# Kernel optimization log

Hardware: AMD Instinct MI355X
Metric: run time of the kernel (lower is better)

Reference implementation:

```python
import jax, jax.numpy as jnp
import numpy as np

DIM = 1024
HEADS = 16
HIDDEN = 4 * DIM

def _gelu_erf(x):
    # GELU via erf, matching the torch module exactly
    return x * 0.5 * (1.0 + jax.lax.erf(x / jnp.sqrt(2.0).astype(x.dtype)))

def setup_inputs() -> dict:
    key = jax.random.key(0)
    ks = jax.random.split(key, 12)
    s = 0.02
    x = jax.random.normal(ks[0], (2, 2048, DIM), dtype=jnp.float32)
    # MHSA params
    ln1_g = jnp.ones((DIM,), jnp.float32)
    ln1_b = jnp.zeros((DIM,), jnp.float32)
    w_qkv = jax.random.normal(ks[1], (DIM, 3 * DIM), jnp.float32) * s  # no bias
    w_proj = jax.random.normal(ks[2], (DIM, DIM), jnp.float32) * s
    b_proj = jnp.zeros((DIM,), jnp.float32)
    # ResMLP params
    ln2_g = jnp.ones((DIM,), jnp.float32)
    ln2_b = jnp.zeros((DIM,), jnp.float32)
    w1 = jax.random.normal(ks[3], (DIM, HIDDEN), jnp.float32) * s
    b1 = jnp.zeros((HIDDEN,), jnp.float32)
    w2 = jax.random.normal(ks[4], (HIDDEN, DIM), jnp.float32) * s
    b2 = jnp.zeros((DIM,), jnp.float32)
    return {"x": x, "ln1_g": ln1_g, "ln1_b": ln1_b, "w_qkv": w_qkv,
            "w_proj": w_proj, "b_proj": b_proj, "ln2_g": ln2_g, "ln2_b": ln2_b,
            "w1": w1, "b1": b1, "w2": w2, "b2": b2}

def _layernorm(x, g, b, eps=1e-5):
    mu = jnp.mean(x, axis=-1, keepdims=True)
    var = jnp.mean(jnp.square(x - mu), axis=-1, keepdims=True)
    return (x - mu) * jax.lax.rsqrt(var + eps) * g + b

def reference(x, ln1_g, ln1_b, w_qkv, w_proj, b_proj, ln2_g, ln2_b, w1, b1, w2, b2):
    B, N, C = x.shape
    H = HEADS
    hd = C // H
    scale = hd ** -0.5
    # --- MHSA (dropout is identity in eval) ---
    h = _layernorm(x, ln1_g, ln1_b)
    qkv = (h @ w_qkv).reshape(B, N, 3, H, hd)
    q = jnp.transpose(qkv[:, :, 0], (0, 2, 1, 3))  # [B,H,N,hd]
    k = jnp.transpose(qkv[:, :, 1], (0, 2, 1, 3))
    v = jnp.transpose(qkv[:, :, 2], (0, 2, 1, 3))
    attn = jax.nn.softmax(jnp.einsum('bhnd,bhmd->bhnm', q, k) * scale, axis=-1)
    out = jnp.einsum('bhnm,bhmd->bhnd', attn, v)
    out = jnp.transpose(out, (0, 2, 1, 3)).reshape(B, N, C)
    x = x + out @ w_proj + b_proj
    # --- ResMLP ---
    h = _layernorm(x, ln2_g, ln2_b)
    h = _gelu_erf(h @ w1 + b1)
    x = x + h @ w2 + b2
    return x
```

## Files before the change

### kernel.cpp

```cpp
#include <hip/hip_runtime.h>
#include <stdint.h>


#define DIMC 1024
#define HIDN 4096
#define SEQ  2048
#define TOK  4096

typedef __bf16 bf16x8 __attribute__((ext_vector_type(8)));
typedef float  f32x4  __attribute__((ext_vector_type(4)));
typedef unsigned short ushort8 __attribute__((ext_vector_type(8)));

__device__ inline unsigned short f2bf(float f) {
  union { float f; unsigned u; } v; v.f = f;
  unsigned u = v.u;
  return (unsigned short)((u + 0x7fffu + ((u >> 16) & 1u)) >> 16);
}

__device__ inline unsigned cvt_pk_bf16(float a, float b) {
  unsigned r;
  asm("v_cvt_pk_bf16_f32 %0, %1, %2" : "=v"(r) : "v"(a), "v"(b));
  return r;
}

#if __has_builtin(__builtin_amdgcn_exp2f)
__device__ inline float fast_exp2(float x) { return __builtin_amdgcn_exp2f(x); }
#else
__device__ inline float fast_exp2(float x) { return exp2f(x); }
#endif

__device__ inline f32x4 mfma_bf16(bf16x8 a, bf16x8 b, f32x4 c) {
  return __builtin_amdgcn_mfma_f32_16x16x32_bf16(a, b, c, 0, 0, 0);
}

typedef const __attribute__((address_space(1))) unsigned int* as1_u32p;
typedef __attribute__((address_space(3))) unsigned int* as3_u32p;
__device__ inline void gload_lds16(const unsigned short* g, unsigned short* l) {
  __builtin_amdgcn_global_load_lds((as1_u32p)(const void*)g, (as3_u32p)(void*)l,
                                   16, 0, 0);
}

__global__ __launch_bounds__(256)
void prep_kernel(const float* __restrict__ wa, unsigned short* __restrict__ ta,
                 const float* __restrict__ wb, unsigned short* __restrict__ tb,
                 const float* __restrict__ wc, unsigned short* __restrict__ tc,
                 const float* __restrict__ wd, unsigned short* __restrict__ td,
                 const float* __restrict__ x, const float* __restrict__ g,
                 const float* __restrict__ bln, unsigned short* __restrict__ out) {
  const int bid = blockIdx.x;
  const int tid = threadIdx.x;
  if (bid < 12288) {
    __shared__ float tile[32][33];
    const float* w; unsigned short* wt; int K, N, bx, by;
    if (bid < 3072)      { w = wa; wt = ta; K = 1024; N = 3072; bx = bid % 96;  by = bid / 96; }
    else if (bid < 4096) { int i = bid - 3072; w = wb; wt = tb; K = 1024; N = 1024; bx = i % 32;  by = i / 32; }
    else if (bid < 8192) { int i = bid - 4096; w = wc; wt = tc; K = 1024; N = 4096; bx = i % 128; by = i / 128; }
    else                 { int i = bid - 8192; w = wd; wt = td; K = 4096; N = 1024; bx = i % 32;  by = i / 32; }
    const int k0 = by * 32;
    const int n0 = bx * 32;
    const int tx = tid & 31;
    const int ty = tid >> 5;
#pragma unroll
    for (int i = 0; i < 4; i++)
      tile[ty + i * 8][tx] = w[(size_t)(k0 + ty + i * 8) * N + n0 + tx];
    __syncthreads();
#pragma unroll
    for (int i = 0; i < 4; i++)
      wt[(size_t)(n0 + ty + i * 8) * K + k0 + tx] = f2bf(tile[tx][ty + i * 8]);
  } else {
    const int row = bid - 12288;
    const float4* xr = (const float4*)&x[(size_t)row * DIMC];
    float4 v = xr[tid];
    float s  = v.x + v.y + v.z + v.w;
    float sq = v.x * v.x + v.y * v.y + v.z * v.z + v.w * v.w;
#pragma unroll
    for (int off = 32; off > 0; off >>= 1) {
      s  += __shfl_xor(s, off, 64);
      sq += __shfl_xor(sq, off, 64);
    }
    __shared__ float red[8];
    if ((tid & 63) == 0) { red[tid >> 6] = s; red[4 + (tid >> 6)] = sq; }
    __syncthreads();
    s  = red[0] + red[1] + red[2] + red[3];
    sq = red[4] + red[5] + red[6] + red[7];
    const float mu  = s * (1.0f / DIMC);
    const float var = sq * (1.0f / DIMC) - mu * mu;
    const float rs  = rsqrtf(var + 1e-5f);
    const int c = tid * 4;
    float vv[4] = {v.x, v.y, v.z, v.w};
#pragma unroll
    for (int j = 0; j < 4; j++)
      out[(size_t)row * DIMC + c + j] = f2bf((vv[j] - mu) * rs * g[c + j] + bln[c + j]);
  }
}

__global__ __launch_bounds__(256)
void ln_kernel(const float* __restrict__ x, const float* __restrict__ g,
               const float* __restrict__ b, unsigned short* __restrict__ out) {
  const int row = blockIdx.x;
  const int tid = threadIdx.x;
  const float4* xr = (const float4*)&x[(size_t)row * DIMC];
  float4 v = xr[tid];
  float s  = v.x + v.y + v.z + v.w;
  float sq = v.x * v.x + v.y * v.y + v.z * v.z + v.w * v.w;
#pragma unroll
  for (int off = 32; off > 0; off >>= 1) {
    s  += __shfl_xor(s, off, 64);
    sq += __shfl_xor(sq, off, 64);
  }
  __shared__ float red[8];
  if ((tid & 63) == 0) { red[tid >> 6] = s; red[4 + (tid >> 6)] = sq; }
  __syncthreads();
  s  = red[0] + red[1] + red[2] + red[3];
  sq = red[4] + red[5] + red[6] + red[7];
  const float mu  = s * (1.0f / DIMC);
  const float var = sq * (1.0f / DIMC) - mu * mu;
  const float rs  = rsqrtf(var + 1e-5f);
  const int c = tid * 4;
  float vv[4] = {v.x, v.y, v.z, v.w};
#pragma unroll
  for (int j = 0; j < 4; j++)
    out[(size_t)row * DIMC + c + j] = f2bf((vv[j] - mu) * rs * g[c + j] + b[c + j]);
}

template <int EPI, int TN>
__global__ __launch_bounds__(256, (TN == 64) ? 4 : 3)
void gemm_bt(const unsigned short* __restrict__ A,
             const unsigned short* __restrict__ Bt,
             float* __restrict__ Cf, unsigned short* __restrict__ Cb,
             const float* __restrict__ bias, const float* __restrict__ res,
             int M, int N, int K,
             unsigned short* __restrict__ qd,
             unsigned short* __restrict__ kTd,
             unsigned short* __restrict__ vd) {
  constexpr int NU = TN / 32;
  constexpr int BP = TN / 32;
  __shared__ unsigned short As[128 * 64];
  __shared__ unsigned short Bs[TN * 64];
  const int gx  = N / TN;
  const int bid = blockIdx.x;
  const int xcd = bid & 7;
  const int lin = bid >> 3;
  const int bx  = lin % gx;
  const int by  = (xcd << 2) + lin / gx;
  const int tid  = threadIdx.x;
  const int lane = tid & 63;
  const int wave = tid >> 6;
  const int m0 = by * 128;
  const int n0 = bx * TN;
  const int wm = (wave >> 1) * 64;
  const int wn = (wave & 1) * (TN / 2);
  const int lm = lane & 15;
  const int lg = lane >> 4;
  const int r8 = tid >> 3;
  const int c8 = tid & 7;
  const int csrc = ((c8 ^ (r8 & 7)) * 8);

  const unsigned short* gA = &A [(size_t)(m0 + r8) * K + csrc];
  const unsigned short* gB = &Bt[(size_t)(n0 + r8) * K + csrc];

  f32x4 acc[4][NU];
#pragma unroll
  for (int t = 0; t < 4; t++)
#pragma unroll
    for (int u = 0; u < NU; u++) acc[t][u] = {0.f, 0.f, 0.f, 0.f};

  const int x0 = (lg ^ (lm & 7)) * 8;
  const int x1 = ((4 + lg) ^ (lm & 7)) * 8;

  for (int k0 = 0; k0 < K; k0 += 64) {
    __syncthreads();
#pragma unroll
    for (int p = 0; p < 4; p++)
      gload_lds16(gA + (size_t)p * 32 * K + k0, &As[p * 2048 + wave * 512]);
#pragma unroll
    for (int p = 0; p < BP; p++)
      gload_lds16(gB + (size_t)p * 32 * K + k0, &Bs[p * 2048 + wave * 512]);
    __syncthreads();
#pragma unroll
    for (int sub = 0; sub < 2; sub++) {
      const int xo = sub ? x1 : x0;
      bf16x8 af[4], bfr[NU];
#pragma unroll
      for (int t = 0; t < 4; t++)  af[t]  = *(const bf16x8*)&As[(wm + t * 16 + lm) * 64 + xo];
#pragma unroll
      for (int u = 0; u < NU; u++) bfr[u] = *(const bf16x8*)&Bs[(wn + u * 16 + lm) * 64 + xo];
#pragma unroll
      for (int t = 0; t < 4; t++)
#pragma unroll
        for (int u = 0; u < NU; u++)
          acc[t][u] = mfma_bf16(af[t], bfr[u], acc[t][u]);
    }
  }

#pragma unroll
  for (int t = 0; t < 4; t++) {
    const int row = m0 + wm + t * 16 + lg * 4;
#pragma unroll
    for (int u = 0; u < NU; u++) {
      const int col = n0 + wn + u * 16 + lm;
#pragma unroll
      for (int r = 0; r < 4; r++) {
        float v = acc[t][u][r];
        size_t idx = (size_t)(row + r) * N + col;
        if (EPI == 0) {
          const int rr = row + r;
          const int bb = rr >> 11, key = rr & (SEQ - 1);
          if (col < 1024) {
            qd[(size_t)rr * 1024 + col] = f2bf(v * 0.18033688011112042f);
          } else if (col < 2048) {
            const int d = col - 1024, h = d >> 6, dd = d & 63;
            kTd[(((size_t)(bb * 16 + h)) * SEQ + key) * 64 + dd] = f2bf(v);
          } else {
            vd[(size_t)rr * 1024 + (col - 2048)] = f2bf(v);
          }
        } else if (EPI == 1) {
          Cf[idx] = v + bias[col] + res[idx];
        } else {
          float xg = v + bias[col];
          Cb[idx] = f2bf(0.5f * xg * (1.0f + erff(xg * 0.70710678118654752f)));
        }
      }
    }
  }
}

__global__ __launch_bounds__(256)
void v_transpose(const unsigned short* __restrict__ vd,
                 unsigned short* __restrict__ vT) {
  const int kt = blockIdx.x;
  const int bh = blockIdx.y;
  const int b = bh >> 4, h = bh & 15;
  const int tid = threadIdx.x;
  __shared__ unsigned short tile[64 * 72];
  const int tok = tid >> 2;
  const int ch  = tid & 3;
  const size_t srow = (size_t)(b * SEQ + kt * 64 + tok) * 1024 + h * 64;
  ushort8 va = *(const ushort8*)&vd[srow + ch * 8];
  ushort8 vb = *(const ushort8*)&vd[srow + 32 + ch * 8];
  *(ushort8*)&tile[tok * 72 + ch * 8] = va;
  *(ushort8*)&tile[tok * 72 + 32 + ch * 8] = vb;
  __syncthreads();
  const int d = tid >> 2;
  ushort8 o0, o1;
#pragma unroll
  for (int j = 0; j < 8; j++) {
    o0[j] = tile[(ch * 8 + j) * 72 + d];
    o1[j] = tile[((ch + 4) * 8 + j) * 72 + d];
  }
  const size_t vdst = ((size_t)bh * 64 + d) * SEQ + kt * 64;
  *(ushort8*)&vT[vdst + ch * 8] = o0;
  *(ushort8*)&vT[vdst + 32 + ch * 8] = o1;
}

__global__ __launch_bounds__(256, 2)
void attn_kernel(const unsigned short* __restrict__ qbuf,
                 const unsigned short* __restrict__ kT,
                 const unsigned short* __restrict__ vT,
                 unsigned short* __restrict__ out) {
  const int bid = blockIdx.x;
  const int xcd = bid & 7;
  const int lin = bid >> 3;
  const int bh  = (xcd << 2) + (lin >> 4);
  const int qt  = lin & 15;
  const int b  = bh >> 4;
  const int h  = bh & 15;
  const int tid  = threadIdx.x;
  const int lane = tid & 63;
  const int wave = tid >> 6;
  const int ks   = wave >> 1;
  const int qh   = wave & 1;
  const int lm = lane & 15;
  const int lg = lane >> 4;

  __shared__ f32x4 shbuf[4096];
  unsigned short* Ks = (unsigned short*)shbuf;
  unsigned short* Vs = (unsigned short*)shbuf + 8192;
  unsigned short* Ps = (unsigned short*)shbuf + 16384;

  const int qrow_base = b * SEQ + qt * 128 + qh * 64;
  bf16x8 qb[4][2];
#pragma unroll
  for (int s = 0; s < 4; s++)
#pragma unroll
    for (int c = 0; c < 2; c++)
      qb[s][c] = *(const bf16x8*)&qbuf[(size_t)(qrow_base + s * 16 + lm) * 1024 +
                                       h * 64 + c * 32 + lg * 8];

  f32x4 o[4][4];
#pragma unroll
  for (int dt = 0; dt < 4; dt++)
#pragma unroll
    for (int s = 0; s < 4; s++) o[dt][s] = {0.f, 0.f, 0.f, 0.f};
  float li[4] = {0.f, 0.f, 0.f, 0.f};

  const unsigned short* kbp = &kT[(size_t)bh * SEQ * 64];
  const unsigned short* vbp = &vT[(size_t)bh * 64 * SEQ];
  const int ts   = tid & 127;
  const int srow = ts >> 3;
  const int slog = ((ts & 7) ^ (srow & 7)) * 8;
  const int koff = ks * 1024;
  const int xk0 = ((lg)     ^ (lm & 7)) * 8;
  const int xk1 = ((4 + lg) ^ (lm & 7)) * 8;
  unsigned short* ksb = Ks + ks * 4096;
  unsigned short* vsb = Vs + ks * 4096;
  unsigned short* psb = Ps + wave * 4096;
  unsigned short* kdst = ksb + ((ts >> 6) * 512);
  unsigned short* vdst = vsb + ((ts >> 6) * 512);

  for (int kt = 0; kt < 16; kt++) {
    __syncthreads();
#pragma unroll
    for (int p = 0; p < 4; p++) {
      gload_lds16(&kbp[(size_t)(koff + kt * 64 + p * 16 + srow) * 64 + slog],
                  kdst + p * 1024);
      gload_lds16(&vbp[(size_t)(p * 16 + srow) * SEQ + koff + kt * 64 + slog],
                  vdst + p * 1024);
    }
    __syncthreads();

#pragma unroll
    for (int u = 0; u < 4; u++) {
      bf16x8 ka0 = *(const bf16x8*)&ksb[(u * 16 + lm) * 64 + xk0];
      bf16x8 ka1 = *(const bf16x8*)&ksb[(u * 16 + lm) * 64 + xk1];
      f32x4 st[4];
#pragma unroll
      for (int s = 0; s < 4; s++) {
        f32x4 z = {0.f, 0.f, 0.f, 0.f};
        z = mfma_bf16(ka0, qb[s][0], z);
        z = mfma_bf16(ka1, qb[s][1], z);
        st[s] = z;
      }
#pragma unroll
      for (int s = 0; s < 4; s++) {
        float p0 = fast_exp2(st[s][0] - 8.0f);
        float p1 = fast_exp2(st[s][1] - 8.0f);
        float p2 = fast_exp2(st[s][2] - 8.0f);
        float p3 = fast_exp2(st[s][3] - 8.0f);
        li[s] += (p0 + p1) + (p2 + p3);
        uint2 pk;
        pk.x = cvt_pk_bf16(p0, p1);
        pk.y = cvt_pk_bf16(p2, p3);
        const int phys = (u * 2 + (lg >> 1)) ^ (lm & 7);
        *(uint2*)&psb[(s * 16 + lm) * 64 + phys * 8 + (lg & 1) * 4] = pk;
      }
    }

#pragma unroll
    for (int kc = 0; kc < 2; kc++) {
      const int xo = kc ? xk1 : xk0;
      bf16x8 pb[4];
#pragma unroll
      for (int s = 0; s < 4; s++)
        pb[s] = *(const bf16x8*)&psb[(s * 16 + lm) * 64 + xo];
#pragma unroll
      for (int dt = 0; dt < 4; dt++) {
        bf16x8 va = *(const bf16x8*)&vsb[(dt * 16 + lm) * 64 + xo];
#pragma unroll
        for (int s = 0; s < 4; s++)
          o[dt][s] = mfma_bf16(va, pb[s], o[dt][s]);
      }
    }
  }

  __syncthreads();
  f32x4* ob = shbuf + qh * 1088;
  float*  lb = (float*)(ob + 1024);
  if (ks == 1) {
#pragma unroll
    for (int dt = 0; dt < 4; dt++)
#pragma unroll
      for (int s = 0; s < 4; s++)
        ob[(dt * 4 + s) * 64 + lane] = o[dt][s];
#pragma unroll
    for (int s = 0; s < 4; s++) lb[s * 64 + lane] = li[s];
  }
  __syncthreads();
  if (ks == 0) {
#pragma unroll
    for (int dt = 0; dt < 4; dt++)
#pragma unroll
      for (int s = 0; s < 4; s++)
        o[dt][s] += ob[(dt * 4 + s) * 64 + lane];
#pragma unroll
    for (int s = 0; s < 4; s++) {
      float l = li[s] + lb[s * 64 + lane];
      l += __shfl_xor(l, 16, 64);
      l += __shfl_xor(l, 32, 64);
      const float inv = 1.0f / l;
#pragma unroll
      for (int dt = 0; dt < 4; dt++) {
        uint2 ok;
        ok.x = cvt_pk_bf16(o[dt][s][0] * inv, o[dt][s][1] * inv);
        ok.y = cvt_pk_bf16(o[dt][s][2] * inv, o[dt][s][3] * inv);
        *(uint2*)&out[(size_t)(qrow_base + s * 16 + lm) * DIMC + h * 64 +
                      dt * 16 + lg * 4] = ok;
      }
    }
  }
}

extern "C" void kernel_launch(void* const* d_in, const int* in_sizes, int n_in,
                              void* d_out, int out_size, void* d_ws, size_t ws_size,
                              hipStream_t stream) {
  const float* x      = (const float*)d_in[0];
  const float* ln1_g  = (const float*)d_in[1];
  const float* ln1_b  = (const float*)d_in[2];
  const float* w_qkv  = (const float*)d_in[3];
  const float* w_proj = (const float*)d_in[4];
  const float* b_proj = (const float*)d_in[5];
  const float* ln2_g  = (const float*)d_in[6];
  const float* ln2_b  = (const float*)d_in[7];
  const float* w1     = (const float*)d_in[8];
  const float* b1     = (const float*)d_in[9];
  const float* w2     = (const float*)d_in[10];
  const float* b2     = (const float*)d_in[11];
  float* out = (float*)d_out;

  char* ws = (char*)d_ws;
  size_t off = 0;
  auto alloc = [&](size_t bytes) { void* p = ws + off; off += (bytes + 255) & ~(size_t)255; return p; };
  unsigned short* wqkvT = (unsigned short*)alloc((size_t)3072 * 1024 * 2);
  unsigned short* wprjT = (unsigned short*)alloc((size_t)1024 * 1024 * 2);
  unsigned short* w1T   = (unsigned short*)alloc((size_t)4096 * 1024 * 2);
  unsigned short* w2T   = (unsigned short*)alloc((size_t)1024 * 4096 * 2);
  unsigned short* hb    = (unsigned short*)alloc((size_t)TOK * 1024 * 2);
  unsigned short* qbuf  = (unsigned short*)alloc((size_t)TOK * 1024 * 2);
  unsigned short* vdb   = (unsigned short*)alloc((size_t)TOK * 1024 * 2);
  unsigned short* attnb = (unsigned short*)alloc((size_t)TOK * 1024 * 2);
  float*          x1    = (float*)         alloc((size_t)TOK * 1024 * 4);
  unsigned short* hidb  = (unsigned short*)alloc((size_t)TOK * 4096 * 2);
  unsigned short* kT = hidb;
  unsigned short* vT = hidb + (size_t)32 * SEQ * 64;

  prep_kernel<<<12288 + TOK, 256, 0, stream>>>(w_qkv, wqkvT, w_proj, wprjT,
                                               w1, w1T, w2, w2T,
                                               x, ln1_g, ln1_b, hb);
  gemm_bt<0, 64><<<1536, 256, 0, stream>>>(
      hb, wqkvT, nullptr, nullptr, nullptr, nullptr, TOK, 3072, 1024,
      qbuf, kT, vdb);
  v_transpose<<<dim3(SEQ / 64, 32), 256, 0, stream>>>(vdb, vT);
  attn_kernel<<<512, 256, 0, stream>>>(qbuf, kT, vT, attnb);
  gemm_bt<1, 64><<<512, 256, 0, stream>>>(
      attnb, wprjT, x1, nullptr, b_proj, x, TOK, 1024, 1024,
      nullptr, nullptr, nullptr);
  ln_kernel<<<TOK, 256, 0, stream>>>(x1, ln2_g, ln2_b, hb);
  gemm_bt<2, 64><<<2048, 256, 0, stream>>>(
      hb, w1T, nullptr, hidb, b1, nullptr, TOK, 4096, 1024,
      nullptr, nullptr, nullptr);
  gemm_bt<1, 64><<<512, 256, 0, stream>>>(
      hidb, w2T, out, nullptr, b2, x1, TOK, 1024, 4096,
      nullptr, nullptr, nullptr);
}
```

Before: 339.6 us.

## Add 256-row wide GEMM, fuse V transpose into QKV epilogue, widen weight prep tiles

Adds a 512-thread gemm_wide kernel with 256x64 tiles for the QKV and FC1 GEMMs, so each B tile is shared across more rows. The QKV epilogue now writes V directly in transposed layout with packed bf16 stores, which removes the separate v_transpose kernel and its intermediate buffer. The weight-conversion prep now uses 64x64 tiles, converts to bf16 before the LDS transpose and uses vectorized loads and stores. gemm_bt drops its unused epilogue paths. The cost is more LDS and a larger register footprint per block, and the transposed V stores are strided.

```diff
diff --git a/kernel.cpp b/kernel.cpp
--- a/kernel.cpp
+++ b/kernel.cpp
@@ -49,26 +49,36 @@
                  const float* __restrict__ bln, unsigned short* __restrict__ out) {
   const int bid = blockIdx.x;
   const int tid = threadIdx.x;
-  if (bid < 12288) {
-    __shared__ float tile[32][33];
+  if (bid < 3072) {
+    __shared__ unsigned short tileS[64 * 68];
     const float* w; unsigned short* wt; int K, N, bx, by;
-    if (bid < 3072)      { w = wa; wt = ta; K = 1024; N = 3072; bx = bid % 96;  by = bid / 96; }
-    else if (bid < 4096) { int i = bid - 3072; w = wb; wt = tb; K = 1024; N = 1024; bx = i % 32;  by = i / 32; }
-    else if (bid < 8192) { int i = bid - 4096; w = wc; wt = tc; K = 1024; N = 4096; bx = i % 128; by = i / 128; }
-    else                 { int i = bid - 8192; w = wd; wt = td; K = 4096; N = 1024; bx = i % 32;  by = i / 32; }
-    const int k0 = by * 32;
-    const int n0 = bx * 32;
-    const int tx = tid & 31;
-    const int ty = tid >> 5;
-#pragma unroll
-    for (int i = 0; i < 4; i++)
-      tile[ty + i * 8][tx] = w[(size_t)(k0 + ty + i * 8) * N + n0 + tx];
-    __syncthreads();
-#pragma unroll
-    for (int i = 0; i < 4; i++)
-      wt[(size_t)(n0 + ty + i * 8) * K + k0 + tx] = f2bf(tile[tx][ty + i * 8]);
+    if (bid < 768)       { w = wa; wt = ta; K = 1024; N = 3072; bx = bid % 48; by = bid / 48; }
+    else if (bid < 1024) { int i = bid - 768;  w = wb; wt = tb; K = 1024; N = 1024; bx = i % 16; by = i / 16; }
+    else if (bid < 2048) { int i = bid - 1024; w = wc; wt = tc; K = 1024; N = 4096; bx = i % 64; by = i / 64; }
+    else                 { int i = bid - 2048; w = wd; wt = td; K = 4096; N = 1024; bx = i % 16; by = i / 16; }
+    const int k0 = by * 64, n0 = bx * 64;
+    const int r  = tid >> 4;
+    const int c4 = tid & 15;
+#pragma unroll
+    for (int it = 0; it < 4; it++) {
+      float4 v = *(const float4*)&w[(size_t)(k0 + r + it * 16) * N + n0 + c4 * 4];
+      ushort4 o;
+      o.x = f2bf(v.x); o.y = f2bf(v.y); o.z = f2bf(v.z); o.w = f2bf(v.w);
+      *(ushort4*)&tileS[(r + it * 16) * 68 + c4 * 4] = o;
+    }
+    __syncthreads();
+#pragma unroll
+    for (int it = 0; it < 4; it++) {
+      const int n = r + it * 16;
+      ushort4 o;
+      o.x = tileS[(c4 * 4 + 0) * 68 + n];
+      o.y = tileS[(c4 * 4 + 1) * 68 + n];
+      o.z = tileS[(c4 * 4 + 2) * 68 + n];
+      o.w = tileS[(c4 * 4 + 3) * 68 + n];
+      *(ushort4*)&wt[(size_t)(n0 + n) * K + k0 + c4 * 4] = o;
+    }
   } else {
-    const int row = bid - 12288;
+    const int row = bid - 3072;
     const float4* xr = (const float4*)&x[(size_t)row * DIMC];
     float4 v = xr[tid];
     float s  = v.x + v.y + v.z + v.w;
@@ -123,16 +133,120 @@
     out[(size_t)row * DIMC + c + j] = f2bf((vv[j] - mu) * rs * g[c + j] + b[c + j]);
 }
 
+template <int EPI>
+__global__ __launch_bounds__(512, 8)
+void gemm_wide(const unsigned short* __restrict__ A,
+               const unsigned short* __restrict__ Bt,
+               unsigned short* __restrict__ Cb,
+               const float* __restrict__ bias,
+               int N, int K,
+               unsigned short* __restrict__ qd,
+               unsigned short* __restrict__ kTd,
+               unsigned short* __restrict__ vT) {
+  __shared__ unsigned short As[256 * 64];
+  __shared__ unsigned short Bs[64 * 64];
+  const int bid = blockIdx.x;
+  const int xcd = bid & 7;
+  const int lin = bid >> 3;
+  const int ii  = lin & 31;
+  const int chunk = lin >> 5;
+  const int bx = chunk * 16 + (ii >> 1);
+  const int by = (xcd << 1) + (ii & 1);
+  const int tid  = threadIdx.x;
+  const int lane = tid & 63;
+  const int wave = tid >> 6;
+  const int m0 = by * 256;
+  const int n0 = bx * 64;
+  const int wm = (wave >> 1) * 64;
+  const int wn = (wave & 1) * 32;
+  const int lm = lane & 15;
+  const int lg = lane >> 4;
+  const int r8 = tid >> 3;
+  const int c8 = tid & 7;
+  const int csrc = (c8 ^ (r8 & 7)) * 8;
+
+  const unsigned short* gA = &A [(size_t)(m0 + r8) * K + csrc];
+  const unsigned short* gB = &Bt[(size_t)(n0 + r8) * K + csrc];
+
+  f32x4 acc[4][2];
+#pragma unroll
+  for (int t = 0; t < 4; t++)
+#pragma unroll
+    for (int u = 0; u < 2; u++) acc[t][u] = {0.f, 0.f, 0.f, 0.f};
+
+  const int x0 = (lg ^ (lm & 7)) * 8;
+  const int x1 = ((4 + lg) ^ (lm & 7)) * 8;
+
+#pragma unroll 1
+  for (int k0 = 0; k0 < K; k0 += 64) {
+    __syncthreads();
+#pragma unroll
+    for (int p = 0; p < 4; p++)
+      gload_lds16(gA + (size_t)p * 64 * K + k0, &As[p * 4096 + wave * 512]);
+    gload_lds16(gB + k0, &Bs[wave * 512]);
+    __syncthreads();
+#pragma unroll
+    for (int sub = 0; sub < 2; sub++) {
+      const int xo = sub ? x1 : x0;
+      bf16x8 af[4], bfr[2];
+#pragma unroll
+      for (int t = 0; t < 4; t++)
+        af[t] = *(const bf16x8*)&As[(wm + t * 16 + lm) * 64 + xo];
+#pragma unroll
+      for (int u = 0; u < 2; u++)
+        bfr[u] = *(const bf16x8*)&Bs[(wn + u * 16 + lm) * 64 + xo];
+#pragma unroll
+      for (int t = 0; t < 4; t++)
+#pragma unroll
+        for (int u = 0; u < 2; u++)
+          acc[t][u] = mfma_bf16(af[t], bfr[u], acc[t][u]);
+    }
+  }
+
+#pragma unroll
+  for (int t = 0; t < 4; t++) {
+    const int row = m0 + wm + t * 16 + lg * 4;
+#pragma unroll
+    for (int u = 0; u < 2; u++) {
+      const int col = n0 + wn + u * 16 + lm;
+      if (EPI == 0 && col >= 2048) {
+        const int d = col - 2048, h = d >> 6, dd = d & 63;
+        const int bb = row >> 11, key = row & (SEQ - 1);
+        uint2 pk;
+        pk.x = cvt_pk_bf16(acc[t][u][0], acc[t][u][1]);
+        pk.y = cvt_pk_bf16(acc[t][u][2], acc[t][u][3]);
+        *(uint2*)&vT[((size_t)((bb << 4) + h) * 64 + dd) * SEQ + key] = pk;
+        continue;
+      }
+#pragma unroll
+      for (int r = 0; r < 4; r++) {
+        float v = acc[t][u][r];
+        if (EPI == 0) {
+          const int rr = row + r;
+          const int bb = rr >> 11, key = rr & (SEQ - 1);
+          if (col < 1024) {
+            qd[(size_t)rr * 1024 + col] = f2bf(v * 0.18033688011112042f);
+          } else {
+            const int d = col - 1024, h = d >> 6, dd = d & 63;
+            kTd[(((size_t)(bb * 16 + h)) * SEQ + key) * 64 + dd] = f2bf(v);
+          }
+        } else {
+          float xg = v + bias[col];
+          Cb[(size_t)(row + r) * N + col] =
+              f2bf(0.5f * xg * (1.0f + erff(xg * 0.70710678118654752f)));
+        }
+      }
+    }
+  }
+}
+
 template <int EPI, int TN>
-__global__ __launch_bounds__(256, (TN == 64) ? 4 : 3)
+__global__ __launch_bounds__(256, 4)
 void gemm_bt(const unsigned short* __restrict__ A,
              const unsigned short* __restrict__ Bt,
              float* __restrict__ Cf, unsigned short* __restrict__ Cb,
              const float* __restrict__ bias, const float* __restrict__ res,
-             int M, int N, int K,
-             unsigned short* __restrict__ qd,
-             unsigned short* __restrict__ kTd,
-             unsigned short* __restrict__ vd) {
+             int M, int N, int K) {
   constexpr int NU = TN / 32;
   constexpr int BP = TN / 32;
   __shared__ unsigned short As[128 * 64];
@@ -168,6 +282,7 @@
   const int x0 = (lg ^ (lm & 7)) * 8;
   const int x1 = ((4 + lg) ^ (lm & 7)) * 8;
 
+#pragma unroll 1
   for (int k0 = 0; k0 < K; k0 += 64) {
     __syncthreads();
 #pragma unroll
@@ -182,9 +297,11 @@
       const int xo = sub ? x1 : x0;
       bf16x8 af[4], bfr[NU];
 #pragma unroll
-      for (int t = 0; t < 4; t++)  af[t]  = *(const bf16x8*)&As[(wm + t * 16 + lm) * 64 + xo];
-#pragma unroll
-      for (int u = 0; u < NU; u++) bfr[u] = *(const bf16x8*)&Bs[(wn + u * 16 + lm) * 64 + xo];
+      for (int t = 0; t < 4; t++)
+        af[t] = *(const bf16x8*)&As[(wm + t * 16 + lm) * 64 + xo];
+#pragma unroll
+      for (int u = 0; u < NU; u++)
+        bfr[u] = *(const bf16x8*)&Bs[(wn + u * 16 + lm) * 64 + xo];
 #pragma unroll
       for (int t = 0; t < 4; t++)
 #pragma unroll
@@ -203,54 +320,10 @@
       for (int r = 0; r < 4; r++) {
         float v = acc[t][u][r];
         size_t idx = (size_t)(row + r) * N + col;
-        if (EPI == 0) {
-          const int rr = row + r;
-          const int bb = rr >> 11, key = rr & (SEQ - 1);
-          if (col < 1024) {
-            qd[(size_t)rr * 1024 + col] = f2bf(v * 0.18033688011112042f);
-          } else if (col < 2048) {
-            const int d = col - 1024, h = d >> 6, dd = d & 63;
-            kTd[(((size_t)(bb * 16 + h)) * SEQ + key) * 64 + dd] = f2bf(v);
-          } else {
-            vd[(size_t)rr * 1024 + (col - 2048)] = f2bf(v);
-          }
-        } else if (EPI == 1) {
-          Cf[idx] = v + bias[col] + res[idx];
-        } else {
-          float xg = v + bias[col];
-          Cb[idx] = f2bf(0.5f * xg * (1.0f + erff(xg * 0.70710678118654752f)));
-        }
-      }
-    }
-  }
-}
-
-__global__ __launch_bounds__(256)
-void v_transpose(const unsigned short* __restrict__ vd,
-                 unsigned short* __restrict__ vT) {
-  const int kt = blockIdx.x;
-  const int bh = blockIdx.y;
-  const int b = bh >> 4, h = bh & 15;
-  const int tid = threadIdx.x;
-  __shared__ unsigned short tile[64 * 72];
-  const int tok = tid >> 2;
-  const int ch  = tid & 3;
-  const size_t srow = (size_t)(b * SEQ + kt * 64 + tok) * 1024 + h * 64;
-  ushort8 va = *(const ushort8*)&vd[srow + ch * 8];
-  ushort8 vb = *(const ushort8*)&vd[srow + 32 + ch * 8];
-  *(ushort8*)&tile[tok * 72 + ch * 8] = va;
-  *(ushort8*)&tile[tok * 72 + 32 + ch * 8] = vb;
-  __syncthreads();
-  const int d = tid >> 2;
-  ushort8 o0, o1;
-#pragma unroll
-  for (int j = 0; j < 8; j++) {
-    o0[j] = tile[(ch * 8 + j) * 72 + d];
-    o1[j] = tile[((ch + 4) * 8 + j) * 72 + d];
-  }
-  const size_t vdst = ((size_t)bh * 64 + d) * SEQ + kt * 64;
-  *(ushort8*)&vT[vdst + ch * 8] = o0;
-  *(ushort8*)&vT[vdst + 32 + ch * 8] = o1;
+        Cf[idx] = v + bias[col] + res[idx];
+      }
+    }
+  }
 }
 
 __global__ __launch_bounds__(256, 2)
@@ -426,29 +499,23 @@
   unsigned short* w2T   = (unsigned short*)alloc((size_t)1024 * 4096 * 2);
   unsigned short* hb    = (unsigned short*)alloc((size_t)TOK * 1024 * 2);
   unsigned short* qbuf  = (unsigned short*)alloc((size_t)TOK * 1024 * 2);
-  unsigned short* vdb   = (unsigned short*)alloc((size_t)TOK * 1024 * 2);
   unsigned short* attnb = (unsigned short*)alloc((size_t)TOK * 1024 * 2);
   float*          x1    = (float*)         alloc((size_t)TOK * 1024 * 4);
   unsigned short* hidb  = (unsigned short*)alloc((size_t)TOK * 4096 * 2);
   unsigned short* kT = hidb;
   unsigned short* vT = hidb + (size_t)32 * SEQ * 64;
 
-  prep_kernel<<<12288 + TOK, 256, 0, stream>>>(w_qkv, wqkvT, w_proj, wprjT,
-                                               w1, w1T, w2, w2T,
-                                               x, ln1_g, ln1_b, hb);
-  gemm_bt<0, 64><<<1536, 256, 0, stream>>>(
-      hb, wqkvT, nullptr, nullptr, nullptr, nullptr, TOK, 3072, 1024,
-      qbuf, kT, vdb);
-  v_transpose<<<dim3(SEQ / 64, 32), 256, 0, stream>>>(vdb, vT);
+  prep_kernel<<<3072 + TOK, 256, 0, stream>>>(w_qkv, wqkvT, w_proj, wprjT,
+                                              w1, w1T, w2, w2T,
+                                              x, ln1_g, ln1_b, hb);
+  gemm_wide<0><<<768, 512, 0, stream>>>(
+      hb, wqkvT, nullptr, nullptr, 3072, 1024, qbuf, kT, vT);
   attn_kernel<<<512, 256, 0, stream>>>(qbuf, kT, vT, attnb);
   gemm_bt<1, 64><<<512, 256, 0, stream>>>(
-      attnb, wprjT, x1, nullptr, b_proj, x, TOK, 1024, 1024,
-      nullptr, nullptr, nullptr);
+      attnb, wprjT, x1, nullptr, b_proj, x, TOK, 1024, 1024);
   ln_kernel<<<TOK, 256, 0, stream>>>(x1, ln2_g, ln2_b, hb);
-  gemm_bt<2, 64><<<2048, 256, 0, stream>>>(
-      hb, w1T, nullptr, hidb, b1, nullptr, TOK, 4096, 1024,
-      nullptr, nullptr, nullptr);
+  gemm_wide<2><<<1024, 512, 0, stream>>>(
+      hb, w1T, hidb, b1, 4096, 1024, nullptr, nullptr, nullptr);
   gemm_bt<1, 64><<<512, 256, 0, stream>>>(
-      hidb, w2T, out, nullptr, b2, x1, TOK, 1024, 4096,
-      nullptr, nullptr, nullptr);
-}
+      hidb, w2T, out, nullptr, b2, x1, TOK, 1024, 4096);
+}
```

Result: slower. 349.3 us (+2.9%).
